# Performance work log

Measured on AMD Instinct MI355X. Metric: run time of the kernel, lower is better.

Reference implementation:

```python
import jax, jax.numpy as jnp
import numpy as np

D_MODEL = 1024
NUM_HEADS = 16
D_K = D_MODEL // NUM_HEADS
THETA = 10000.0
B, S = 2, 2048


def apply_rope(x, token_position, theta=THETA):
    # x: [B, H, S, d_k]; token_position: [B, S] int
    d_k = x.shape[-1]
    inv_freq = 1.0 / theta ** (jnp.arange(0, d_k, 2, dtype=jnp.float32) / d_k)  # [d_k/2]
    angles = token_position.astype(jnp.float32)[:, :, None] * inv_freq[None, None, :]  # [B,S,d_k/2]
    cos = jnp.cos(angles)[:, None, :, :]  # [B,1,S,d_k/2]
    sin = jnp.sin(angles)[:, None, :, :]
    x_even = x[..., 0::2]
    x_odd = x[..., 1::2]
    rot_even = x_even * cos - x_odd * sin
    rot_odd = x_even * sin + x_odd * cos
    # interleave back: stack on new last axis, then flatten
    return jnp.stack([rot_even, rot_odd], axis=-1).reshape(x.shape)


def setup_inputs() -> dict:
    key = jax.random.key(0)
    kx, kq, kk, kv, ko = jax.random.split(key, 5)
    scale = 1.0 / np.sqrt(D_MODEL)
    x = jax.random.normal(kx, (B, S, D_MODEL), dtype=jnp.float32)
    WQ = jax.random.normal(kq, (D_MODEL, D_MODEL), dtype=jnp.float32) * scale
    WK = jax.random.normal(kk, (D_MODEL, D_MODEL), dtype=jnp.float32) * scale
    WV = jax.random.normal(kv, (D_MODEL, D_MODEL), dtype=jnp.float32) * scale
    WO = jax.random.normal(ko, (D_MODEL, D_MODEL), dtype=jnp.float32) * scale
    token_position = jnp.broadcast_to(jnp.arange(S, dtype=jnp.int32)[None, :], (B, S))
    return {"x": x, "token_position": token_position, "WQ": WQ, "WK": WK, "WV": WV, "WO": WO}


def reference(x, token_position, WQ, WK, WV, WO):
    Batch, seq, _ = x.shape
    Q = jnp.einsum('bsd,de->bse', x, WQ).reshape(Batch, seq, NUM_HEADS, D_K).transpose(0, 2, 1, 3)
    K = jnp.einsum('bsd,de->bse', x, WK).reshape(Batch, seq, NUM_HEADS, D_K).transpose(0, 2, 1, 3)
    V = jnp.einsum('bsd,de->bse', x, WV).reshape(Batch, seq, NUM_HEADS, D_K).transpose(0, 2, 1, 3)
    Q = apply_rope(Q, token_position)
    K = apply_rope(K, token_position)
    score = jnp.einsum('bhqd,bhkd->bhqk', Q, K) / jnp.sqrt(jnp.float32(D_K))
    causal = jnp.tril(jnp.ones((seq, seq), dtype=bool))  # [S,S]
    score = jnp.where(causal[None, None, :, :], score, -jnp.inf)
    probs = jax.nn.softmax(score, axis=-1)
    out = jnp.einsum('bhqk,bhkd->bhqd', probs, V)
    out = out.transpose(0, 2, 1, 3).reshape(Batch, seq, D_MODEL)
    return jnp.einsum('bsd,de->bse', out, WO)
```

## Files before the change

kernel.cpp:

```cpp
#include <hip/hip_runtime.h>
#include <hip/hip_bf16.h>

typedef __attribute__((ext_vector_type(8))) short short8;
typedef __attribute__((ext_vector_type(4))) float f32x4;
typedef __hip_bfloat16 bf16_t;

#define SEQ 2048
#define DM 1024
#define NH 16
#define DK 64

static __device__ __forceinline__ f32x4 mfma16x16x32(short8 a, short8 b, f32x4 c) {
  return __builtin_amdgcn_mfma_f32_16x16x32_bf16(a, b, c, 0, 0, 0);
}

__global__ void sniff_dtype(const unsigned int* __restrict__ x, int* __restrict__ flag) {
  int lane = threadIdx.x & 63;
  int cnt = 0;
  for (int r = 0; r < 4; ++r) {
    unsigned int v = x[lane + r * 64];
    int e = (v >> 7) & 0xFF;
    if (e >= 100 && e <= 145) cnt++;
  }
  for (int d = 1; d < 64; d <<= 1) cnt += __shfl_xor(cnt, d, 64);
  if (lane == 0) *flag = (cnt >= 192) ? 1 : 0;
}

__global__ __launch_bounds__(256) void convert_x(const void* __restrict__ src,
                                                 bf16_t* __restrict__ dst,
                                                 const int* __restrict__ flag, int n4) {
  int f = *flag;
  int i = blockIdx.x * blockDim.x + threadIdx.x;
  if (i >= n4) return;
  if (f) {
    ((uint2*)dst)[i] = ((const uint2*)src)[i];
  } else {
    const float4 v = ((const float4*)src)[i];
    bf16_t o[4] = {__float2bfloat16(v.x), __float2bfloat16(v.y),
                   __float2bfloat16(v.z), __float2bfloat16(v.w)};
    ((uint2*)dst)[i] = *(const uint2*)o;
  }
}

__global__ __launch_bounds__(256) void transpose_w(const void* __restrict__ w0,
                                                   const void* __restrict__ w1,
                                                   const void* __restrict__ w2,
                                                   const void* __restrict__ w3,
                                                   bf16_t* __restrict__ wt_base,
                                                   const int* __restrict__ flag) {
  int f = *flag;
  const void* src = (blockIdx.z == 0) ? w0 : (blockIdx.z == 1) ? w1
                  : (blockIdx.z == 2) ? w2 : w3;
  bf16_t* dst = wt_base + (size_t)((blockIdx.z + 1) & 3) * DM * DM;
  __shared__ bf16_t tile[64][65];
  int t = threadIdx.x;
  int tx = t & 63, ty = t >> 6;
  int r0 = blockIdx.y * 64, c0 = blockIdx.x * 64;
  for (int i = 0; i < 64; i += 4) {
    size_t idx = (size_t)(r0 + ty + i) * DM + c0 + tx;
    tile[ty + i][tx] = f ? ((const bf16_t*)src)[idx]
                         : __float2bfloat16(((const float*)src)[idx]);
  }
  __syncthreads();
  for (int i = 0; i < 64; i += 4)
    dst[(size_t)(c0 + ty + i) * DM + r0 + tx] = tile[tx][ty + i];
}

__global__ __launch_bounds__(256) void build_rope_tab(const int* __restrict__ tokpos,
                                                      float2* __restrict__ tab) {
  int i = blockIdx.x * 256 + threadIdx.x;
  int m = i >> 5, pp = i & 31;
  float pos = (float)tokpos[m];
  float invf = __powf(10000.0f, -(float)pp * (1.0f / 32.0f));
  float sn, cs;
  sincosf(pos * invf, &sn, &cs);
  tab[i] = make_float2(cs, sn);
}

__global__ __launch_bounds__(256) void gemm128_qkv(const bf16_t* __restrict__ A,
                                                   const bf16_t* __restrict__ WTqkv,
                                                   bf16_t* __restrict__ Qb,
                                                   bf16_t* __restrict__ Kb,
                                                   bf16_t* __restrict__ VTo,
                                                   const float2* __restrict__ rtab) {
  __shared__ __align__(16) char smem[36864];
  bf16_t (*As)[72] = (bf16_t(*)[72])smem;
  bf16_t (*Bs)[72] = (bf16_t(*)[72])(smem + 18432);
  int t = threadIdx.x;
  int w = t >> 6, lane = t & 63, l15 = lane & 15, quad = lane >> 4;
  int wrow = w >> 1, wcol = w & 1;
  int m0 = blockIdx.y * 128, nx = blockIdx.x, n0 = nx * 128;
  int srow = t >> 1, scol = (t & 1) * 32;
  const bf16_t* ag = A + (size_t)(m0 + srow) * DM + scol;
  const bf16_t* bg = WTqkv + (size_t)(n0 + srow) * DM + scol;
  f32x4 acc[4][4] = {};
  for (int kk = 0; kk < DM; kk += 64) {
    short8 a0 = *(const short8*)(ag + kk);
    short8 a1 = *(const short8*)(ag + kk + 8);
    short8 a2 = *(const short8*)(ag + kk + 16);
    short8 a3 = *(const short8*)(ag + kk + 24);
    short8 b0 = *(const short8*)(bg + kk);
    short8 b1 = *(const short8*)(bg + kk + 8);
    short8 b2 = *(const short8*)(bg + kk + 16);
    short8 b3 = *(const short8*)(bg + kk + 24);
    __syncthreads();
    *(short8*)&As[srow][scol] = a0;       *(short8*)&As[srow][scol + 8] = a1;
    *(short8*)&As[srow][scol + 16] = a2;  *(short8*)&As[srow][scol + 24] = a3;
    *(short8*)&Bs[srow][scol] = b0;       *(short8*)&Bs[srow][scol + 8] = b1;
    *(short8*)&Bs[srow][scol + 16] = b2;  *(short8*)&Bs[srow][scol + 24] = b3;
    __syncthreads();
    short8 af[4][2], bfr[4][2];
#pragma unroll
    for (int mt = 0; mt < 4; ++mt) {
      af[mt][0] = *(const short8*)&As[wrow * 64 + mt * 16 + l15][quad * 8];
      af[mt][1] = *(const short8*)&As[wrow * 64 + mt * 16 + l15][32 + quad * 8];
    }
#pragma unroll
    for (int nt = 0; nt < 4; ++nt) {
      bfr[nt][0] = *(const short8*)&Bs[wcol * 64 + nt * 16 + l15][quad * 8];
      bfr[nt][1] = *(const short8*)&Bs[wcol * 64 + nt * 16 + l15][32 + quad * 8];
    }
#pragma unroll
    for (int mt = 0; mt < 4; ++mt)
#pragma unroll
      for (int nt = 0; nt < 4; ++nt) {
        acc[mt][nt] = mfma16x16x32(af[mt][0], bfr[nt][0], acc[mt][nt]);
        acc[mt][nt] = mfma16x16x32(af[mt][1], bfr[nt][1], acc[mt][nt]);
      }
  }

  int sel = nx >> 3;
  int nc = (nx & 7) * 128;
  if (sel < 2) {
    bf16_t* dst = sel ? Kb : Qb;
    int h = (nc >> 6) + wcol;
    float sgnv = (l15 & 1) ? 1.0f : -1.0f;
#pragma unroll
    for (int mt = 0; mt < 4; ++mt)
#pragma unroll
      for (int r = 0; r < 4; ++r) {
        int m = m0 + wrow * 64 + mt * 16 + quad * 4 + r;
        int b = m >> 11, s = m & (SEQ - 1);
        const float2* tr = rtab + m * 32;
        bf16_t* dp = dst + (((size_t)(b * NH + h)) * SEQ + s) * DK;
#pragma unroll
        for (int nt = 0; nt < 4; ++nt) {
          int d = nt * 16 + l15;
          float val = acc[mt][nt][r];
          float partner = __shfl_xor(val, 1, 64);
          float2 cssn = tr[d >> 1];
          dp[d] = __float2bfloat16(val * cssn.x + sgnv * partner * cssn.y);
        }
      }
  } else {
    __syncthreads();
    bf16_t (*Tw)[72] = (bf16_t(*)[72])(smem + w * 9216);
#pragma unroll
    for (int mt = 0; mt < 4; ++mt)
#pragma unroll
      for (int nt = 0; nt < 4; ++nt)
#pragma unroll
        for (int r = 0; r < 4; ++r)
          Tw[nt * 16 + l15][mt * 16 + quad * 4 + r] = __float2bfloat16(acc[mt][nt][r]);
    int b = m0 >> 11, s_base = m0 & (SEQ - 1);
    int h = (nc >> 6) + wcol;
#pragma unroll
    for (int c = 0; c < 4; ++c) {
      int d = c * 16 + (lane >> 2);
      int s2 = (lane & 3) * 16;
      size_t ob = ((size_t)(b * NH + h) * DK + d) * SEQ + s_base + wrow * 64 + s2;
      *(short8*)&VTo[ob] = *(const short8*)&Tw[d][s2];
      *(short8*)&VTo[ob + 8] = *(const short8*)&Tw[d][s2 + 8];
    }
  }
}

__global__ __launch_bounds__(256) void gemm128_out(const bf16_t* __restrict__ A,
                                                   const bf16_t* __restrict__ BT,
                                                   void* __restrict__ out,
                                                   const int* __restrict__ flag) {
  __shared__ __align__(16) bf16_t As[128][72];
  __shared__ __align__(16) bf16_t Bs[128][72];
  int f = *flag;
  int t = threadIdx.x;
  int w = t >> 6, lane = t & 63, l15 = lane & 15, quad = lane >> 4;
  int wrow = w >> 1, wcol = w & 1;
  int m0 = blockIdx.y * 128, n0 = blockIdx.x * 128;
  int srow = t >> 1, scol = (t & 1) * 32;
  const bf16_t* ag = A + (size_t)(m0 + srow) * DM + scol;
  const bf16_t* bg = BT + (size_t)(n0 + srow) * DM + scol;
  f32x4 acc[4][4] = {};
  for (int kk = 0; kk < DM; kk += 64) {
    short8 a0 = *(const short8*)(ag + kk);
    short8 a1 = *(const short8*)(ag + kk + 8);
    short8 a2 = *(const short8*)(ag + kk + 16);
    short8 a3 = *(const short8*)(ag + kk + 24);
    short8 b0 = *(const short8*)(bg + kk);
    short8 b1 = *(const short8*)(bg + kk + 8);
    short8 b2 = *(const short8*)(bg + kk + 16);
    short8 b3 = *(const short8*)(bg + kk + 24);
    __syncthreads();
    *(short8*)&As[srow][scol] = a0;       *(short8*)&As[srow][scol + 8] = a1;
    *(short8*)&As[srow][scol + 16] = a2;  *(short8*)&As[srow][scol + 24] = a3;
    *(short8*)&Bs[srow][scol] = b0;       *(short8*)&Bs[srow][scol + 8] = b1;
    *(short8*)&Bs[srow][scol + 16] = b2;  *(short8*)&Bs[srow][scol + 24] = b3;
    __syncthreads();
    short8 af[4][2], bfr[4][2];
#pragma unroll
    for (int mt = 0; mt < 4; ++mt) {
      af[mt][0] = *(const short8*)&As[wrow * 64 + mt * 16 + l15][quad * 8];
      af[mt][1] = *(const short8*)&As[wrow * 64 + mt * 16 + l15][32 + quad * 8];
    }
#pragma unroll
    for (int nt = 0; nt < 4; ++nt) {
      bfr[nt][0] = *(const short8*)&Bs[wcol * 64 + nt * 16 + l15][quad * 8];
      bfr[nt][1] = *(const short8*)&Bs[wcol * 64 + nt * 16 + l15][32 + quad * 8];
    }
#pragma unroll
    for (int mt = 0; mt < 4; ++mt)
#pragma unroll
      for (int nt = 0; nt < 4; ++nt) {
        acc[mt][nt] = mfma16x16x32(af[mt][0], bfr[nt][0], acc[mt][nt]);
        acc[mt][nt] = mfma16x16x32(af[mt][1], bfr[nt][1], acc[mt][nt]);
      }
  }
#pragma unroll
  for (int mt = 0; mt < 4; ++mt)
#pragma unroll
    for (int nt = 0; nt < 4; ++nt)
#pragma unroll
      for (int r = 0; r < 4; ++r) {
        int m = m0 + wrow * 64 + mt * 16 + quad * 4 + r;
        int col = n0 + wcol * 64 + nt * 16 + l15;
        size_t oidx = (size_t)m * DM + col;
        if (f) ((bf16_t*)out)[oidx] = __float2bfloat16(acc[mt][nt][r]);
        else   ((float*)out)[oidx] = acc[mt][nt][r];
      }
}

__global__ __launch_bounds__(256) void attn_fwd(const bf16_t* __restrict__ Q,
                                                const bf16_t* __restrict__ K,
                                                const bf16_t* __restrict__ VT,
                                                bf16_t* __restrict__ O) {
  int x = blockIdx.x, bh = blockIdx.y;
  int b = bh >> 4, h = bh & 15;
  int raw = (x + bh) & 31;
  int oct = raw >> 3, off = raw & 7;
  int p = (oct == 0) ? off : (oct == 1) ? (15 - off) : (oct == 2) ? (16 + off) : (31 - off);
  int t = threadIdx.x;
  int w = t >> 6, lane = t & 63, l15 = lane & 15, quad = lane >> 4;
  const size_t base = (size_t)bh * SEQ * DK;
  const bf16_t* Qp = Q + base;
  const bf16_t* Kp = K + base;
  const bf16_t* VTp = VT + base;

  __shared__ __align__(16) bf16_t Ks[64][72];
  __shared__ __align__(16) bf16_t Vs[64][72];
  __shared__ __align__(16) bf16_t Pb[4][16][72];

  int row = p * 64 + w * 16 + l15;
  short8 qf0 = *(const short8*)(Qp + (size_t)row * DK + quad * 8);
  short8 qf1 = *(const short8*)(Qp + (size_t)row * DK + 32 + quad * 8);

  int srow = t >> 2, scoff = (t & 3) * 16;
  const bf16_t* kst = Kp + (size_t)srow * DK + scoff;
  const bf16_t* vst = VTp + (size_t)srow * SEQ + scoff;

  short8 kA = *(const short8*)(kst);
  short8 kB = *(const short8*)(kst + 8);
  short8 vA = *(const short8*)(vst);
  short8 vB = *(const short8*)(vst + 8);

  f32x4 o[4] = {};
  float r[4] = {0.f, 0.f, 0.f, 0.f};

  for (int kb = 0; kb <= p; ++kb) {
    __syncthreads();
    *(short8*)&Ks[srow][scoff] = kA;
    *(short8*)&Ks[srow][scoff + 8] = kB;
    *(short8*)&Vs[srow][scoff] = vA;
    *(short8*)&Vs[srow][scoff + 8] = vB;
    __syncthreads();

    int nkb = (kb < p) ? (kb + 1) : p;
    kA = *(const short8*)(kst + (size_t)nkb * 64 * DK);
    kB = *(const short8*)(kst + (size_t)nkb * 64 * DK + 8);
    vA = *(const short8*)(vst + (size_t)nkb * 64);
    vB = *(const short8*)(vst + (size_t)nkb * 64 + 8);

    short8 kf0[4], kf1[4];
#pragma unroll
    for (int kt = 0; kt < 4; ++kt) {
      kf0[kt] = *(const short8*)&Ks[kt * 16 + l15][quad * 8];
      kf1[kt] = *(const short8*)&Ks[kt * 16 + l15][32 + quad * 8];
    }

    f32x4 sc[4];
#pragma unroll
    for (int kt = 0; kt < 4; ++kt) {
      f32x4 a = {};
      a = mfma16x16x32(qf0, kf0[kt], a);
      a = mfma16x16x32(qf1, kf1[kt], a);
      sc[kt] = a;
    }

    bool diag = (kb == p);
#pragma unroll
    for (int kt = 0; kt < 4; ++kt)
#pragma unroll
      for (int reg = 0; reg < 4; ++reg) {
        float sv = sc[kt][reg] * 0.125f;
        if (diag) {
          int kg = kt * 16 + l15, qg = w * 16 + quad * 4 + reg;
          if (kg > qg) sv = -30000.0f;
        }
        float pp = __expf(sv);
        r[reg] += pp;
        Pb[w][quad * 4 + reg][kt * 16 + l15] = __float2bfloat16(pp);
      }

    short8 p0 = *(const short8*)&Pb[w][l15][quad * 8];
    short8 p1 = *(const short8*)&Pb[w][l15][32 + quad * 8];
#pragma unroll
    for (int dt = 0; dt < 4; ++dt) {
      short8 vf0 = *(const short8*)&Vs[dt * 16 + l15][quad * 8];
      short8 vf1 = *(const short8*)&Vs[dt * 16 + l15][32 + quad * 8];
      o[dt] = mfma16x16x32(p0, vf0, o[dt]);
      o[dt] = mfma16x16x32(p1, vf1, o[dt]);
    }
  }

  for (int d = 1; d < 16; d <<= 1)
#pragma unroll
    for (int reg = 0; reg < 4; ++reg)
      r[reg] += __shfl_xor(r[reg], d, 64);

#pragma unroll
  for (int dt = 0; dt < 4; ++dt)
#pragma unroll
    for (int reg = 0; reg < 4; ++reg) {
      int col = h * DK + dt * 16 + l15;
      int q = p * 64 + w * 16 + quad * 4 + reg;
      O[((size_t)b * SEQ + q) * DM + col] = __float2bfloat16(o[dt][reg] / r[reg]);
    }
}

extern "C" void kernel_launch(void* const* d_in, const int* in_sizes, int n_in,
                              void* d_out, int out_size, void* d_ws, size_t ws_size,
                              hipStream_t stream) {
  const void* x = d_in[0];
  const int* tokpos = (const int*)d_in[1];
  const void* WQ = d_in[2];
  const void* WK = d_in[3];
  const void* WV = d_in[4];
  const void* WO = d_in[5];

  char* ws = (char*)d_ws;
  const size_t MB = 1024 * 1024;
  bf16_t* WT  = (bf16_t*)ws;
  bf16_t* Xc  = (bf16_t*)(ws + 8 * MB);
  bf16_t* Qb  = (bf16_t*)(ws + 16 * MB);
  bf16_t* Kb  = (bf16_t*)(ws + 24 * MB);
  bf16_t* VTb = (bf16_t*)(ws + 32 * MB);
  bf16_t* Ab  = (bf16_t*)(ws + 8 * MB);
  int* flag   = (int*)(ws + 40 * MB);
  float2* rtab = (float2*)(ws + 41 * MB);

  dim3 blk(256);
  sniff_dtype<<<1, 64, 0, stream>>>((const unsigned int*)x, flag);
  convert_x<<<4096, blk, 0, stream>>>(x, Xc, flag, (SEQ * 2 * DM) / 4);
  transpose_w<<<dim3(16, 16, 4), blk, 0, stream>>>(WQ, WK, WV, WO, WT, flag);
  build_rope_tab<<<512, blk, 0, stream>>>(tokpos, rtab);
  gemm128_qkv<<<dim3(24, 32), blk, 0, stream>>>(Xc, WT + (size_t)DM * DM, Qb, Kb, VTb, rtab);
  attn_fwd<<<dim3(32, 32), blk, 0, stream>>>(Qb, Kb, VTb, Ab);
  gemm128_out<<<dim3(8, 32), blk, 0, stream>>>(Ab, WT, d_out, flag);
}
```

Baseline: 209.6 us.

## Merge preprocessing kernels into one launch and stage Q/K stores through LDS

Three small preprocessing kernels (x conversion, weight transpose, RoPE table) are merged into one kernel that dispatches on block index, removing two launches and the gaps between them. Separately, the Q/K epilogue of the QKV GEMM now writes its RoPE-rotated results into shared memory first and then issues 16-byte vectorized global stores, instead of scattered 2-byte stores. The cost is an extra __syncthreads and LDS round trip in the epilogue, plus a larger, branchier prep kernel whose every block reserves the transpose tile.

```diff
diff --git a/kernel.cpp b/kernel.cpp
--- a/kernel.cpp
+++ b/kernel.cpp
@@ -26,55 +26,53 @@
   if (lane == 0) *flag = (cnt >= 192) ? 1 : 0;
 }
 
-__global__ __launch_bounds__(256) void convert_x(const void* __restrict__ src,
-                                                 bf16_t* __restrict__ dst,
-                                                 const int* __restrict__ flag, int n4) {
+__global__ __launch_bounds__(256) void prep(const void* __restrict__ x,
+                                            bf16_t* __restrict__ Xc,
+                                            const void* __restrict__ w0,
+                                            const void* __restrict__ w1,
+                                            const void* __restrict__ w2,
+                                            const void* __restrict__ w3,
+                                            bf16_t* __restrict__ wt_base,
+                                            const int* __restrict__ tokpos,
+                                            float2* __restrict__ rtab,
+                                            const int* __restrict__ flag) {
   int f = *flag;
-  int i = blockIdx.x * blockDim.x + threadIdx.x;
-  if (i >= n4) return;
-  if (f) {
-    ((uint2*)dst)[i] = ((const uint2*)src)[i];
+  int bx = blockIdx.x, t = threadIdx.x;
+  __shared__ bf16_t tile[64][65];
+  if (bx < 4096) {
+    int i = bx * 256 + t;
+    if (f) {
+      ((uint2*)Xc)[i] = ((const uint2*)x)[i];
+    } else {
+      const float4 v = ((const float4*)x)[i];
+      bf16_t o[4] = {__float2bfloat16(v.x), __float2bfloat16(v.y),
+                     __float2bfloat16(v.z), __float2bfloat16(v.w)};
+      ((uint2*)Xc)[i] = *(const uint2*)o;
+    }
+  } else if (bx < 5120) {
+    int rem = bx - 4096;
+    int z = rem >> 8, bxx = rem & 15, byy = (rem >> 4) & 15;
+    const void* src = (z == 0) ? w0 : (z == 1) ? w1 : (z == 2) ? w2 : w3;
+    bf16_t* dst = wt_base + (size_t)((z + 1) & 3) * DM * DM;
+    int tx = t & 63, ty = t >> 6;
+    int r0 = byy * 64, c0 = bxx * 64;
+    for (int i = 0; i < 64; i += 4) {
+      size_t idx = (size_t)(r0 + ty + i) * DM + c0 + tx;
+      tile[ty + i][tx] = f ? ((const bf16_t*)src)[idx]
+                           : __float2bfloat16(((const float*)src)[idx]);
+    }
+    __syncthreads();
+    for (int i = 0; i < 64; i += 4)
+      dst[(size_t)(c0 + ty + i) * DM + r0 + tx] = tile[tx][ty + i];
   } else {
-    const float4 v = ((const float4*)src)[i];
-    bf16_t o[4] = {__float2bfloat16(v.x), __float2bfloat16(v.y),
-                   __float2bfloat16(v.z), __float2bfloat16(v.w)};
-    ((uint2*)dst)[i] = *(const uint2*)o;
-  }
-}
-
-__global__ __launch_bounds__(256) void transpose_w(const void* __restrict__ w0,
-                                                   const void* __restrict__ w1,
-                                                   const void* __restrict__ w2,
-                                                   const void* __restrict__ w3,
-                                                   bf16_t* __restrict__ wt_base,
-                                                   const int* __restrict__ flag) {
-  int f = *flag;
-  const void* src = (blockIdx.z == 0) ? w0 : (blockIdx.z == 1) ? w1
-                  : (blockIdx.z == 2) ? w2 : w3;
-  bf16_t* dst = wt_base + (size_t)((blockIdx.z + 1) & 3) * DM * DM;
-  __shared__ bf16_t tile[64][65];
-  int t = threadIdx.x;
-  int tx = t & 63, ty = t >> 6;
-  int r0 = blockIdx.y * 64, c0 = blockIdx.x * 64;
-  for (int i = 0; i < 64; i += 4) {
-    size_t idx = (size_t)(r0 + ty + i) * DM + c0 + tx;
-    tile[ty + i][tx] = f ? ((const bf16_t*)src)[idx]
-                         : __float2bfloat16(((const float*)src)[idx]);
-  }
-  __syncthreads();
-  for (int i = 0; i < 64; i += 4)
-    dst[(size_t)(c0 + ty + i) * DM + r0 + tx] = tile[tx][ty + i];
-}
-
-__global__ __launch_bounds__(256) void build_rope_tab(const int* __restrict__ tokpos,
-                                                      float2* __restrict__ tab) {
-  int i = blockIdx.x * 256 + threadIdx.x;
-  int m = i >> 5, pp = i & 31;
-  float pos = (float)tokpos[m];
-  float invf = __powf(10000.0f, -(float)pp * (1.0f / 32.0f));
-  float sn, cs;
-  sincosf(pos * invf, &sn, &cs);
-  tab[i] = make_float2(cs, sn);
+    int i = (bx - 5120) * 256 + t;
+    int m = i >> 5, pp = i & 31;
+    float pos = (float)tokpos[m];
+    float invf = __powf(10000.0f, -(float)pp * (1.0f / 32.0f));
+    float sn, cs;
+    sincosf(pos * invf, &sn, &cs);
+    rtab[i] = make_float2(cs, sn);
+  }
 }
 
 __global__ __launch_bounds__(256) void gemm128_qkv(const bf16_t* __restrict__ A,
@@ -131,30 +129,37 @@
 
   int sel = nx >> 3;
   int nc = (nx & 7) * 128;
+  __syncthreads();
+  bf16_t (*Tw)[72] = (bf16_t(*)[72])(smem + w * 9216);
+  int b = m0 >> 11;
+  int h = (nc >> 6) + wcol;
   if (sel < 2) {
     bf16_t* dst = sel ? Kb : Qb;
-    int h = (nc >> 6) + wcol;
     float sgnv = (l15 & 1) ? 1.0f : -1.0f;
 #pragma unroll
     for (int mt = 0; mt < 4; ++mt)
 #pragma unroll
       for (int r = 0; r < 4; ++r) {
         int m = m0 + wrow * 64 + mt * 16 + quad * 4 + r;
-        int b = m >> 11, s = m & (SEQ - 1);
         const float2* tr = rtab + m * 32;
-        bf16_t* dp = dst + (((size_t)(b * NH + h)) * SEQ + s) * DK;
 #pragma unroll
         for (int nt = 0; nt < 4; ++nt) {
           int d = nt * 16 + l15;
           float val = acc[mt][nt][r];
           float partner = __shfl_xor(val, 1, 64);
           float2 cssn = tr[d >> 1];
-          dp[d] = __float2bfloat16(val * cssn.x + sgnv * partner * cssn.y);
+          Tw[mt * 16 + quad * 4 + r][d] = __float2bfloat16(val * cssn.x + sgnv * partner * cssn.y);
         }
       }
+    int s_base = (m0 & (SEQ - 1)) + wrow * 64;
+    bf16_t* dq = dst + ((size_t)(b * NH + h) * SEQ + s_base) * DK;
+#pragma unroll
+    for (int c = 0; c < 8; ++c) {
+      int row = c * 8 + (lane >> 3);
+      int col = (lane & 7) * 8;
+      *(short8*)&dq[(size_t)row * DK + col] = *(const short8*)&Tw[row][col];
+    }
   } else {
-    __syncthreads();
-    bf16_t (*Tw)[72] = (bf16_t(*)[72])(smem + w * 9216);
 #pragma unroll
     for (int mt = 0; mt < 4; ++mt)
 #pragma unroll
@@ -162,8 +167,7 @@
 #pragma unroll
         for (int r = 0; r < 4; ++r)
           Tw[nt * 16 + l15][mt * 16 + quad * 4 + r] = __float2bfloat16(acc[mt][nt][r]);
-    int b = m0 >> 11, s_base = m0 & (SEQ - 1);
-    int h = (nc >> 6) + wcol;
+    int s_base = m0 & (SEQ - 1);
 #pragma unroll
     for (int c = 0; c < 4; ++c) {
       int d = c * 16 + (lane >> 2);
@@ -368,9 +372,7 @@
 
   dim3 blk(256);
   sniff_dtype<<<1, 64, 0, stream>>>((const unsigned int*)x, flag);
-  convert_x<<<4096, blk, 0, stream>>>(x, Xc, flag, (SEQ * 2 * DM) / 4);
-  transpose_w<<<dim3(16, 16, 4), blk, 0, stream>>>(WQ, WK, WV, WO, WT, flag);
-  build_rope_tab<<<512, blk, 0, stream>>>(tokpos, rtab);
+  prep<<<5632, blk, 0, stream>>>(x, Xc, WQ, WK, WV, WO, WT, tokpos, rtab, flag);
   gemm128_qkv<<<dim3(24, 32), blk, 0, stream>>>(Xc, WT + (size_t)DM * DM, Qb, Kb, VTb, rtab);
   attn_fwd<<<dim3(32, 32), blk, 0, stream>>>(Qb, Kb, VTb, Ab);
   gemm128_out<<<dim3(8, 32), blk, 0, stream>>>(Ab, WT, d_out, flag);
```

New measurement: 213.1 us. No clear change (+1.7%).
